# Performance work log

Measured on AMD Instinct MI355X. Metric: run time of the kernel, lower is better.

Reference implementation:

```python
import jax, jax.numpy as jnp
import numpy as np

EPS = 1e-8

def _gn1(x, w, b):
    # GroupNorm(num_groups=1): normalize each sample over (C, T), per-channel affine.
    mean = jnp.mean(x, axis=(1, 2), keepdims=True)
    var = jnp.mean((x - mean) ** 2, axis=(1, 2), keepdims=True)
    xn = (x - mean) * jax.lax.rsqrt(var + EPS)
    return xn * w[None, :, None] + b[None, :, None]

def _film(h, e, gw, gb, bw, bb):
    # gamma/beta: Linear -> ReLU (dropout is identity in eval), broadcast over time.
    gamma = jax.nn.relu(e @ gw.T + gb)  # [B, C]
    beta = jax.nn.relu(e @ bw.T + bb)   # [B, C]
    return gamma[:, :, None] * h + beta[:, :, None]

def setup_inputs() -> dict:
    key = jax.random.key(0)
    ks = jax.random.split(key, 16)
    B, C, T = 16, 256, 16000
    s = lambda k, shape, scale: jax.random.normal(k, shape, dtype=jnp.float32) * scale
    return {
        "x": s(ks[0], (B, C, T), 1.0),
        "cue": s(ks[1], (B, 512), 1.0),
        "gn_a_w": jnp.ones((C,), jnp.float32), "gn_a_b": jnp.zeros((C,), jnp.float32),
        "gn_n_w": jnp.ones((C,), jnp.float32), "gn_n_b": jnp.zeros((C,), jnp.float32),
        "f1g_w": s(ks[2], (C, 512), 0.04), "f1g_b": jnp.zeros((C,), jnp.float32),
        "f1b_w": s(ks[3], (C, 512), 0.04), "f1b_b": jnp.zeros((C,), jnp.float32),
        "ln1_w": jnp.ones((C,), jnp.float32), "ln1_b": jnp.zeros((C,), jnp.float32),
        "conv1_w": s(ks[4], (128, C), 0.06),
        "cds_w": s(ks[5], (256, 512), 0.04),
        "f2g_w": s(ks[6], (128, 256), 0.06), "f2g_b": jnp.zeros((128,), jnp.float32),
        "f2b_w": s(ks[7], (128, 256), 0.06), "f2b_b": jnp.zeros((128,), jnp.float32),
        "ln2_w": jnp.ones((128,), jnp.float32), "ln2_b": jnp.zeros((128,), jnp.float32),
        "conv2_w": s(ks[8], (256, 128), 0.08),
    }

def reference(x, cue, gn_a_w, gn_a_b, gn_n_w, gn_n_b, f1g_w, f1g_b, f1b_w, f1b_b,
              ln1_w, ln1_b, conv1_w, cds_w, f2g_w, f2g_b, f2b_w, f2b_b,
              ln2_w, ln2_b, conv2_w):
    x = _gn1(x, gn_a_w, gn_a_b)                 # norm_audio (GroupNorm(1, C))
    x = _gn1(x, gn_n_w, gn_n_b)                 # norm (GroupNorm(1, C))
    x = _film(x, cue, f1g_w, f1g_b, f1b_w, f1b_b) + x  # film1 + residual
    x = _gn1(x, ln1_w, ln1_b)                   # layer_norm1
    x = jnp.einsum('bct,oc->bot', x, conv1_w)   # 1x1 Conv1d, no bias -> [B,128,T]
    cue2 = jax.nn.relu(cue @ cds_w.T)           # cue_down_sample2 -> [B,256]
    x = _film(x, cue2, f2g_w, f2g_b, f2b_w, f2b_b) + x  # film2 + residual
    x = _gn1(x, ln2_w, ln2_b)                   # layer_norm2
    x = jnp.einsum('bct,oc->bot', x, conv2_w)   # 1x1 Conv1d -> [B,256,T]
    return x
```

## Files before the change

### kernel.cpp

```cpp
#include <hip/hip_runtime.h>
#include <hip/hip_bf16.h>
#include <hip/hip_fp16.h>

#define T_LEN   16000
#define NB      16
#define NTT     250
#define NTB     125
#define EPSV    1e-8f

typedef _Float16 f16x8 __attribute__((ext_vector_type(8)));
typedef float    f32x4 __attribute__((ext_vector_type(4)));

__device__ __forceinline__ ushort f2h(float f) {
    _Float16 h = (_Float16)f;
    return *(ushort*)&h;
}
__device__ __forceinline__ float f4c(const float4& v, int i) {
    return i == 0 ? v.x : i == 1 ? v.y : i == 2 ? v.z : v.w;
}
__device__ __forceinline__ void gld16(const ushort* g, ushort* l) {
    __builtin_amdgcn_global_load_lds(
        (const __attribute__((address_space(1))) uint*)g,
        (__attribute__((address_space(3))) uint*)l, 16, 0, 0);
}
__device__ __forceinline__ float waveRed64(float v) {
    #pragma unroll
    for (int m = 1; m <= 32; m <<= 1) v += __shfl_xor(v, m, 64);
    return v;
}
__device__ __forceinline__ float4 ntload4(const float* p) {
    f32x4 v = __builtin_nontemporal_load((const f32x4*)p);
    return make_float4(v[0], v[1], v[2], v[3]);
}

__device__ __forceinline__ float blockSum256(float v, float* red)
{
    #pragma unroll
    for (int off = 32; off; off >>= 1) v += __shfl_down(v, off, 64);
    __syncthreads();
    if ((threadIdx.x & 63) == 0) red[threadIdx.x >> 6] = v;
    __syncthreads();
    return red[0] + red[1] + red[2] + red[3];
}

__global__ __launch_bounds__(256) void kP1F(
    const float* __restrict__ x, ushort* __restrict__ Xp,
    float* __restrict__ sp, float* __restrict__ qp,
    const float* __restrict__ cue,
    const float* __restrict__ f1g_w, const float* __restrict__ f1g_b,
    const float* __restrict__ f1b_w, const float* __restrict__ f1b_b,
    const float* __restrict__ cds_w,
    float* __restrict__ G1, float* __restrict__ B1, float* __restrict__ CUE2)
{
    const int bid = blockIdx.x;
    if (bid < 256) {
        const int c = bid;
        const int lane = threadIdx.x & 63, w = threadIdx.x >> 6;
        const float4 wg0 = *(const float4*)(f1g_w + c*512 + lane*8);
        const float4 wg1 = *(const float4*)(f1g_w + c*512 + lane*8 + 4);
        const float4 wb0 = *(const float4*)(f1b_w + c*512 + lane*8);
        const float4 wb1 = *(const float4*)(f1b_w + c*512 + lane*8 + 4);
        const float4 wc0 = *(const float4*)(cds_w + c*512 + lane*8);
        const float4 wc1 = *(const float4*)(cds_w + c*512 + lane*8 + 4);
        #pragma unroll
        for (int bb = 0; bb < 4; ++bb) {
            const int b = w*4 + bb;
            const float4 u0 = *(const float4*)(cue + b*512 + lane*8);
            const float4 u1 = *(const float4*)(cue + b*512 + lane*8 + 4);
            float g = 0.f, bt = 0.f, cv = 0.f;
            #pragma unroll
            for (int i = 0; i < 4; ++i) {
                g  = fmaf(f4c(u0,i), f4c(wg0,i), g);  g  = fmaf(f4c(u1,i), f4c(wg1,i), g);
                bt = fmaf(f4c(u0,i), f4c(wb0,i), bt); bt = fmaf(f4c(u1,i), f4c(wb1,i), bt);
                cv = fmaf(f4c(u0,i), f4c(wc0,i), cv); cv = fmaf(f4c(u1,i), f4c(wc1,i), cv);
            }
            g = waveRed64(g); bt = waveRed64(bt); cv = waveRed64(cv);
            if (lane == 0) {
                G1[b*256 + c]   = fmaxf(g + f1g_b[c], 0.f) + 1.f;
                B1[b*256 + c]   = fmaxf(bt + f1b_b[c], 0.f);
                CUE2[b*256 + c] = fmaxf(cv, 0.f);
            }
        }
        return;
    }

    const int pb = bid - 256;
    const int b = pb / NTT, tt = pb % NTT;
    const int t0 = tt * 64;
    const int tid = threadIdx.x;
    const int cq = tid >> 2, jq = tid & 3;
    __shared__ __align__(16) ushort Hs[256][68];

    #pragma unroll
    for (int cc = 0; cc < 4; ++cc) {
        const int c = cc*64 + cq;
        float s4 = 0.f, q4 = 0.f;
        #pragma unroll
        for (int i = 0; i < 4; ++i) {
            const int ts = (jq + i*4)*4;
            const float4 v = ntload4(x + ((size_t)(b*256 + c))*T_LEN + t0 + ts);
            s4 += v.x + v.y + v.z + v.w;
            q4 += v.x*v.x + v.y*v.y + v.z*v.z + v.w*v.w;
            const ushort h0 = f2h(v.x), h1 = f2h(v.y), h2 = f2h(v.z), h3 = f2h(v.w);
            uint2 pk;
            pk.x = (uint)h0 | ((uint)h1 << 16);
            pk.y = (uint)h2 | ((uint)h3 << 16);
            *(uint2*)&Hs[c][ts] = pk;
        }
        s4 += __shfl_xor(s4, 1, 4); s4 += __shfl_xor(s4, 2, 4);
        q4 += __shfl_xor(q4, 1, 4); q4 += __shfl_xor(q4, 2, 4);
        if (jq == 0) {
            sp[((size_t)b*NTT + tt)*256 + c] = s4;
            qp[((size_t)b*NTT + tt)*256 + c] = q4;
        }
    }
    __syncthreads();
    ushort* dst = Xp + ((size_t)(b*NTT + tt)*4)*4096;
    #pragma unroll
    for (int k = 0; k < 8; ++k) {
        const int d  = tid + k*256;
        const int kc = d >> 9, r = d & 511;
        const int t  = r >> 3, us = r & 7;
        const int u  = us ^ (t & 7);
        const int c0 = kc*64 + u*8;
        uint4 val;
        val.x = (uint)Hs[c0+0][t] | ((uint)Hs[c0+1][t] << 16);
        val.y = (uint)Hs[c0+2][t] | ((uint)Hs[c0+3][t] << 16);
        val.z = (uint)Hs[c0+4][t] | ((uint)Hs[c0+5][t] << 16);
        val.w = (uint)Hs[c0+6][t] | ((uint)Hs[c0+7][t] << 16);
        *(uint4*)(dst + (size_t)d*8) = val;
    }
}

__global__ __launch_bounds__(256) void kR_reduce(
    const float* __restrict__ sp, const float* __restrict__ qp,
    float* __restrict__ s1, float* __restrict__ q1)
{
    const int cg = blockIdx.x, b = blockIdx.y;
    const int ci = threadIdx.x & 31, ig = threadIdx.x >> 5;
    const int c = cg*32 + ci;
    float s = 0.f, q = 0.f;
    for (int i = ig; i < NTT; i += 8) {
        s += sp[((size_t)b*NTT + i)*256 + c];
        q += qp[((size_t)b*NTT + i)*256 + c];
    }
    __shared__ float rs[8][32], rq[8][32];
    rs[ig][ci] = s; rq[ig][ci] = q;
    __syncthreads();
    if (threadIdx.x < 32) {
        float ss = 0.f, qq = 0.f;
        #pragma unroll
        for (int g = 0; g < 8; ++g) { ss += rs[g][threadIdx.x]; qq += rq[g][threadIdx.x]; }
        s1[b*256 + cg*32 + threadIdx.x] = ss;
        q1[b*256 + cg*32 + threadIdx.x] = qq;
    }
}

__global__ __launch_bounds__(256) void kM2F(
    const float* __restrict__ s1, const float* __restrict__ q1,
    const float* __restrict__ gn_a_w, const float* __restrict__ gn_a_b,
    const float* __restrict__ gn_n_w, const float* __restrict__ gn_n_b,
    const float* __restrict__ G1, const float* __restrict__ B1,
    const float* __restrict__ ln1_w, const float* __restrict__ ln1_b,
    const float* __restrict__ CUE2,
    const float* __restrict__ f2g_w, const float* __restrict__ f2g_b,
    const float* __restrict__ f2b_w, const float* __restrict__ f2b_b,
    const float* __restrict__ conv1_w,
    float* __restrict__ a4o, float* __restrict__ G2,
    float* __restrict__ E, ushort* __restrict__ Msf)
{
    const int og = blockIdx.x, b = blockIdx.y;
    const int c = threadIdx.x;
    __shared__ float red[4];
    __shared__ float sc2[256], sa4[256], sd4[256], sg2[16];

    const float sc = s1[b*256 + c];
    const float qc = q1[b*256 + c];

    const float Ninv = 1.f / (256.f * 16000.f);
    const float Tf = 16000.f;

    float S  = blockSum256(sc, red);
    float Q  = blockSum256(qc, red);
    float mu1 = S * Ninv;
    float var1 = Q * Ninv - mu1 * mu1;
    float r1 = rsqrtf(var1 + EPSV);
    float a1 = gn_a_w[c] * r1;
    float d1 = gn_a_b[c] - mu1 * r1 * gn_a_w[c];

    float S2 = blockSum256(a1*sc + Tf*d1, red);
    float Q2 = blockSum256(a1*a1*qc + 2.f*a1*d1*sc + Tf*d1*d1, red);
    float mu2 = S2 * Ninv;
    float var2 = Q2 * Ninv - mu2 * mu2;
    float r2 = rsqrtf(var2 + EPSV);
    float wn = gn_n_w[c];
    float a2 = wn * r2 * a1;
    float d2 = wn * r2 * (d1 - mu2) + gn_n_b[c];

    const float g1v = G1[b*256 + c];
    const float b1v = B1[b*256 + c];
    float a3 = g1v * a2;
    float d3 = g1v * d2 + b1v;

    float S3 = blockSum256(a3*sc + Tf*d3, red);
    float Q3 = blockSum256(a3*a3*qc + 2.f*a3*d3*sc + Tf*d3*d3, red);
    float mu3 = S3 * Ninv;
    float var3 = Q3 * Ninv - mu3 * mu3;
    float r3 = rsqrtf(var3 + EPSV);
    float w1 = ln1_w[c];
    const float a4v = w1 * r3 * a3;
    const float d4v = w1 * r3 * (d3 - mu3) + ln1_b[c];
    sa4[c] = a4v;
    sd4[c] = d4v;
    if (og == 0) a4o[b*256 + c] = a4v;
    sc2[c] = CUE2[b*256 + c];
    __syncthreads();

    const int oi = c >> 4, l16 = c & 15;
    const int o = og*16 + oi;
    float g = 0.f, bt = 0.f, ed = 0.f;
    #pragma unroll
    for (int q = 0; q < 4; ++q) {
        const int k0 = l16*16 + q*4;
        const float4 a  = *(const float4*)(f2g_w  + o*256 + k0);
        const float4 bb = *(const float4*)(f2b_w  + o*256 + k0);
        const float4 cc = *(const float4*)(conv1_w + o*256 + k0);
        const float4 u  = *(const float4*)(&sc2[k0]);
        const float4 dd = *(const float4*)(&sd4[k0]);
        #pragma unroll
        for (int i = 0; i < 4; ++i) {
            g  = fmaf(f4c(u,i),  f4c(a,i),  g);
            bt = fmaf(f4c(u,i),  f4c(bb,i), bt);
            ed = fmaf(f4c(dd,i), f4c(cc,i), ed);
        }
    }
    #pragma unroll
    for (int m = 1; m <= 8; m <<= 1) {
        g  += __shfl_xor(g, m, 16);
        bt += __shfl_xor(bt, m, 16);
        ed += __shfl_xor(ed, m, 16);
    }
    if (l16 == 0) {
        const float G2v = fmaxf(g + f2g_b[o], 0.f) + 1.f;
        const float B2v = fmaxf(bt + f2b_b[o], 0.f);
        G2[b*128 + o] = G2v;
        E[b*128 + o]  = G2v * ed + B2v;
        sg2[oi] = G2v;
    }
    __syncthreads();
    const float av = sa4[c];
    #pragma unroll
    for (int i = 0; i < 16; ++i) {
        const int oo = og*16 + i;
        Msf[((size_t)b*128 + oo)*256 + c] = f2h(sg2[i] * conv1_w[oo*256 + c] * av);
    }
}

__global__ __launch_bounds__(256) void kC_gemm(
    const ushort* __restrict__ Xp, const ushort* __restrict__ Msf,
    const float* __restrict__ E,
    float* __restrict__ q2p)
{
    const int tb = blockIdx.x, b = blockIdx.y;
    const int tid = threadIdx.x, lane = tid & 63, w = tid >> 6;
    const int wo = w >> 1, wt = w & 1;
    const int sub = lane >> 4, li = lane & 15;
    const int o0 = wo * 64;
    __shared__ __align__(16) ushort Bs[32768];
    __shared__ float sQp[2][128];

    const ushort* src = Xp + ((size_t)(b*NTT + 2*tb)*4)*4096;
    const ushort* mp  = Msf + (size_t)b*128*256;

    f32x4 acc[4][4];
    #pragma unroll
    for (int i = 0; i < 4; ++i)
        #pragma unroll
        for (int jx = 0; jx < 4; ++jx) acc[i][jx] = (f32x4){0.f,0.f,0.f,0.f};

    #pragma unroll
    for (int m = 0; m < 16; ++m) {
        const int off = m*2048 + w*512;
        gld16(src + off + lane*8, &Bs[off]);
    }
    __syncthreads();

    #pragma unroll
    for (int ks = 0; ks < 8; ++ks) {
        const int kc = ks >> 1;
        const int uo = (ks & 1)*4 + sub;
        f16x8 xf[4];
        #pragma unroll
        for (int ft = 0; ft < 4; ++ft) {
            const int tl = ft*16 + li;
            xf[ft] = *(const f16x8*)&Bs[(wt*4 + kc)*4096 + tl*64 + (uo ^ (tl & 7))*8];
        }
        const int k8 = kc*64 + (ks & 1)*32 + 8*sub;
        #pragma unroll
        for (int fo = 0; fo < 4; ++fo) {
            const f16x8 mf = *(const f16x8*)(mp + (size_t)(o0 + fo*16 + li)*256 + k8);
            #pragma unroll
            for (int ft = 0; ft < 4; ++ft)
                acc[ft][fo] = __builtin_amdgcn_mfma_f32_16x16x32_f16(xf[ft], mf, acc[ft][fo], 0, 0, 0);
        }
    }

    #pragma unroll
    for (int fo = 0; fo < 4; ++fo) {
        const int o = o0 + fo*16 + li;
        const float ev = E[b*128 + o];
        float qv = 0.f;
        #pragma unroll
        for (int ft = 0; ft < 4; ++ft)
            #pragma unroll
            for (int r = 0; r < 4; ++r) {
                const float z = acc[ft][fo][r] + ev;
                qv += z*z;
            }
        qv += __shfl_xor(qv, 16, 64); qv += __shfl_xor(qv, 32, 64);
        if (sub == 0) sQp[wt][o] = qv;
    }
    __syncthreads();
    if (tid < 128)
        q2p[((size_t)b*NTB + tb)*128 + tid] = sQp[0][tid] + sQp[1][tid];
}

__global__ __launch_bounds__(256) void kD2_buildF(
    const float* __restrict__ q2p,
    const float* __restrict__ ln2_w, const float* __restrict__ ln2_b,
    const float* __restrict__ Ev,
    const float* __restrict__ a4, const float* __restrict__ G2,
    const float* __restrict__ s1,
    const float* __restrict__ conv1_w, const float* __restrict__ conv2_w,
    ushort* __restrict__ Fsf, float* __restrict__ h)
{
    const int b = blockIdx.y, pg = blockIdx.x;
    const int tid = threadIdx.x;
    __shared__ float Qs[32][128];
    __shared__ float sA2[128], sAE[128], sAS[256];
    __shared__ float rS[2], rQ[2];

    sAS[tid] = a4[b*256 + tid] * s1[b*256 + tid];
    __syncthreads();

    float s2v = 0.f, qq = 0.f;
    if (tid < 128) {
        float dot = 0.f;
        #pragma unroll 4
        for (int c4 = 0; c4 < 64; ++c4) {
            const float4 cw = *(const float4*)(conv1_w + tid*256 + c4*4);
            const float4 as = *(const float4*)(&sAS[c4*4]);
            dot = fmaf(cw.x, as.x, dot); dot = fmaf(cw.y, as.y, dot);
            dot = fmaf(cw.z, as.z, dot); dot = fmaf(cw.w, as.w, dot);
        }
        s2v = G2[b*128 + tid] * dot + 16000.f * Ev[b*128 + tid];
        for (int tb = 0; tb < NTB; ++tb)
            qq += q2p[((size_t)b*NTB + tb)*128 + tid];
        float S = s2v, Q = qq;
        #pragma unroll
        for (int off = 32; off; off >>= 1) {
            S += __shfl_down(S, off, 64);
            Q += __shfl_down(Q, off, 64);
        }
        if ((tid & 63) == 0) { rS[tid >> 6] = S; rQ[tid >> 6] = Q; }
    }
    __syncthreads();
    const float N2inv = 1.f / (128.f * 16000.f);
    const float mu  = (rS[0] + rS[1]) * N2inv;
    const float var = (rQ[0] + rQ[1]) * N2inv - mu * mu;
    const float r = rsqrtf(var + EPSV);
    if (tid < 128) {
        const float a2v = ln2_w[tid] * r;
        const float d2v = ln2_b[tid] - mu * ln2_w[tid] * r;
        sA2[tid] = a2v;
        sAE[tid] = a2v * Ev[b*128 + tid] + d2v;
    }
    __syncthreads();

    #pragma unroll
    for (int k = 0; k < 16; ++k) {
        const int idx = tid + k*256;
        const int p = idx >> 7, o = idx & 127;
        Qs[p][o] = conv2_w[(pg*32 + p)*128 + o] * sA2[o] * G2[b*128 + o];
    }
    __syncthreads();
    float acc[32];
    #pragma unroll
    for (int p = 0; p < 32; ++p) acc[p] = 0.f;
    for (int o = 0; o < 128; ++o) {
        const float mv = conv1_w[o*256 + tid];
        #pragma unroll
        for (int p = 0; p < 32; ++p) acc[p] = fmaf(Qs[p][o], mv, acc[p]);
    }
    const float a = a4[b*256 + tid];
    #pragma unroll
    for (int p = 0; p < 32; ++p) {
        const size_t idx = ((size_t)b*256 + pg*32 + p)*256 + tid;
        Fsf[idx] = f2h(acc[p] * a);
    }
    if (tid < 32) {
        const int p = pg*32 + tid;
        float hv = 0.f;
        for (int o = 0; o < 128; ++o)
            hv += conv2_w[p*128 + o] * sAE[o];
        h[b*256 + p] = hv;
    }
}

__global__ __launch_bounds__(256) void kE_gemm(
    const ushort* __restrict__ Xp, const ushort* __restrict__ Fsf,
    const float* __restrict__ h, float* __restrict__ out)
{
    const int txp = blockIdx.x;
    const int b = blockIdx.y >> 1;
    const int o_base = (blockIdx.y & 1) * 128;
    const int tid = threadIdx.x, lane = tid & 63, w = tid >> 6;
    const int sub = lane >> 4, li = lane & 15;
    const int o0 = o_base + w * 32;
    __shared__ __align__(16) ushort Bs[2][16384];

    const ushort* fp = Fsf + (size_t)b*65536;

    f16x8 ff[8][2];
    #pragma unroll
    for (int ks = 0; ks < 8; ++ks) {
        const int k8 = (ks >> 1)*64 + (ks & 1)*32 + 8*sub;
        #pragma unroll
        for (int fo = 0; fo < 2; ++fo)
            ff[ks][fo] = *(const f16x8*)(fp + (size_t)(o0 + fo*16 + li)*256 + k8);
    }
    float hv[2];
    #pragma unroll
    for (int fo = 0; fo < 2; ++fo)
        hv[fo] = h[b*256 + o0 + fo*16 + li];

    const ushort* src0 = Xp + ((size_t)(b*NTT + 2*txp)*4)*4096;

    #pragma unroll
    for (int m = 0; m < 8; ++m) {
        const int off = m*2048 + w*512;
        gld16(src0 + off + lane*8, &Bs[0][off]);
    }
    __syncthreads();

    #pragma unroll
    for (int tile = 0; tile < 2; ++tile) {
        if (tile == 0) {
            const ushort* src1 = src0 + 16384;
            #pragma unroll
            for (int m = 0; m < 8; ++m) {
                const int off = m*2048 + w*512;
                gld16(src1 + off + lane*8, &Bs[1][off]);
            }
        }
        f32x4 acc[4][2];
        #pragma unroll
        for (int i = 0; i < 4; ++i)
            #pragma unroll
            for (int jx = 0; jx < 2; ++jx) acc[i][jx] = (f32x4){0.f,0.f,0.f,0.f};

        #pragma unroll
        for (int ks = 0; ks < 8; ++ks) {
            const int kc = ks >> 1;
            const int uo = (ks & 1)*4 + sub;
            f16x8 xf[4];
            #pragma unroll
            for (int ft = 0; ft < 4; ++ft) {
                const int tl = ft*16 + li;
                xf[ft] = *(const f16x8*)&Bs[tile][kc*4096 + tl*64 + (uo ^ (tl & 7))*8];
            }
            #pragma unroll
            for (int fo = 0; fo < 2; ++fo)
                #pragma unroll
                for (int ft = 0; ft < 4; ++ft)
                    acc[ft][fo] = __builtin_amdgcn_mfma_f32_16x16x32_f16(xf[ft], ff[ks][fo], acc[ft][fo], 0, 0, 0);
        }

        const int t0 = (2*txp + tile)*64;
        #pragma unroll
        for (int fo = 0; fo < 2; ++fo) {
            const int o = o0 + fo*16 + li;
            float* obase = out + ((size_t)(b*256 + o))*T_LEN + t0;
            #pragma unroll
            for (int ft = 0; ft < 4; ++ft) {
                f32x4 v;
                v[0] = acc[ft][fo][0] + hv[fo];
                v[1] = acc[ft][fo][1] + hv[fo];
                v[2] = acc[ft][fo][2] + hv[fo];
                v[3] = acc[ft][fo][3] + hv[fo];
                __builtin_nontemporal_store(v, (f32x4*)(obase + ft*16 + sub*4));
            }
        }
        if (tile == 0) __syncthreads();
    }
}

extern "C" void kernel_launch(void* const* d_in, const int* in_sizes, int n_in,
                              void* d_out, int out_size, void* d_ws, size_t ws_size,
                              hipStream_t stream)
{
    const float* x       = (const float*)d_in[0];
    const float* cue     = (const float*)d_in[1];
    const float* gn_a_w  = (const float*)d_in[2];
    const float* gn_a_b  = (const float*)d_in[3];
    const float* gn_n_w  = (const float*)d_in[4];
    const float* gn_n_b  = (const float*)d_in[5];
    const float* f1g_w   = (const float*)d_in[6];
    const float* f1g_b   = (const float*)d_in[7];
    const float* f1b_w   = (const float*)d_in[8];
    const float* f1b_b   = (const float*)d_in[9];
    const float* ln1_w   = (const float*)d_in[10];
    const float* ln1_b   = (const float*)d_in[11];
    const float* conv1_w = (const float*)d_in[12];
    const float* cds_w   = (const float*)d_in[13];
    const float* f2g_w   = (const float*)d_in[14];
    const float* f2g_b   = (const float*)d_in[15];
    const float* f2b_w   = (const float*)d_in[16];
    const float* f2b_b   = (const float*)d_in[17];
    const float* ln2_w   = (const float*)d_in[18];
    const float* ln2_b   = (const float*)d_in[19];
    const float* conv2_w = (const float*)d_in[20];
    float* out = (float*)d_out;

    float* ws = (float*)d_ws;
    float*  sp   = ws;
    float*  qp   = ws + 1024000;
    float*  G1   = ws + 2048000;
    float*  B1   = ws + 2052096;
    float*  CUE2 = ws + 2056192;
    float*  G2   = ws + 2060288;
    float*  a4   = ws + 2062336;
    float*  E    = ws + 2066432;
    float*  h    = ws + 2068480;
    float*  s1   = ws + 2072576;
    float*  q1   = ws + 2076672;
    float*  q2p  = ws + 2080768;
    ushort* Msf  = (ushort*)(ws + 2336768);
    ushort* Fsf  = (ushort*)(ws + 2598912);
    ushort* Xp   = (ushort*)(ws + 3123200);

    kP1F<<<256 + NTT*NB, 256, 0, stream>>>(x, Xp, sp, qp,
        cue, f1g_w, f1g_b, f1b_w, f1b_b, cds_w, G1, B1, CUE2);

    kR_reduce<<<dim3(8, NB), 256, 0, stream>>>(sp, qp, s1, q1);

    kM2F<<<dim3(8, NB), 256, 0, stream>>>(s1, q1,
        gn_a_w, gn_a_b, gn_n_w, gn_n_b, G1, B1, ln1_w, ln1_b,
        CUE2, f2g_w, f2g_b, f2b_w, f2b_b, conv1_w,
        a4, G2, E, Msf);

    kC_gemm<<<dim3(NTB, NB), 256, 0, stream>>>(Xp, Msf, E, q2p);

    kD2_buildF<<<dim3(8, NB), 256, 0, stream>>>(q2p, ln2_w, ln2_b, E,
                                                a4, G2, s1, conv1_w, conv2_w,
                                                Fsf, h);

    kE_gemm<<<dim3(NTB, NB*2), 256, 0, stream>>>(Xp, Fsf, h, out);
}
```

Baseline: 293.2 us.

## Keep GEMM weights in registers and double-buffer two X tiles in kC_gemm

kC_gemm now gives each wave 32 output channels across both time tiles instead of 64 channels on one tile. The wave preloads its whole Msf weight slice into registers once rather than reloading it per k-step from global memory. The second 64-step X tile is loaded into a separate LDS buffer while the first is computed, and the per-wave partial sums are written straight to q2p without the shared reduction. This trades more register pressure (16 f16x8 weight vectors held live) for fewer global weight loads and overlap of the second tile's load with compute.

Measured after the change: 271.3 us. 7.5% less time.

```diff
diff --git a/kernel.cpp b/kernel.cpp
--- a/kernel.cpp
+++ b/kernel.cpp
@@ -261,68 +261,90 @@
     const float* __restrict__ E,
     float* __restrict__ q2p)
 {
-    const int tb = blockIdx.x, b = blockIdx.y;
+    const int tp = blockIdx.x, b = blockIdx.y;
     const int tid = threadIdx.x, lane = tid & 63, w = tid >> 6;
-    const int wo = w >> 1, wt = w & 1;
     const int sub = lane >> 4, li = lane & 15;
-    const int o0 = wo * 64;
-    __shared__ __align__(16) ushort Bs[32768];
-    __shared__ float sQp[2][128];
-
-    const ushort* src = Xp + ((size_t)(b*NTT + 2*tb)*4)*4096;
-    const ushort* mp  = Msf + (size_t)b*128*256;
-
-    f32x4 acc[4][4];
-    #pragma unroll
-    for (int i = 0; i < 4; ++i)
-        #pragma unroll
-        for (int jx = 0; jx < 4; ++jx) acc[i][jx] = (f32x4){0.f,0.f,0.f,0.f};
-
-    #pragma unroll
-    for (int m = 0; m < 16; ++m) {
+    const int o0 = w * 32;
+    __shared__ __align__(16) ushort Bs[2][16384];
+
+    const ushort* mp = Msf + (size_t)b*32768;
+
+    f16x8 mf[8][2];
+    #pragma unroll
+    for (int ks = 0; ks < 8; ++ks) {
+        const int k8 = (ks >> 1)*64 + (ks & 1)*32 + 8*sub;
+        #pragma unroll
+        for (int fo = 0; fo < 2; ++fo)
+            mf[ks][fo] = *(const f16x8*)(mp + (size_t)(o0 + fo*16 + li)*256 + k8);
+    }
+    float ev[2];
+    #pragma unroll
+    for (int fo = 0; fo < 2; ++fo)
+        ev[fo] = E[b*128 + o0 + fo*16 + li];
+
+    const ushort* src0 = Xp + ((size_t)(b*NTT + 2*tp)*4)*4096;
+
+    #pragma unroll
+    for (int m = 0; m < 8; ++m) {
         const int off = m*2048 + w*512;
-        gld16(src + off + lane*8, &Bs[off]);
-    }
-    __syncthreads();
-
-    #pragma unroll
-    for (int ks = 0; ks < 8; ++ks) {
-        const int kc = ks >> 1;
-        const int uo = (ks & 1)*4 + sub;
-        f16x8 xf[4];
-        #pragma unroll
-        for (int ft = 0; ft < 4; ++ft) {
-            const int tl = ft*16 + li;
-            xf[ft] = *(const f16x8*)&Bs[(wt*4 + kc)*4096 + tl*64 + (uo ^ (tl & 7))*8];
-        }
-        const int k8 = kc*64 + (ks & 1)*32 + 8*sub;
-        #pragma unroll
-        for (int fo = 0; fo < 4; ++fo) {
-            const f16x8 mf = *(const f16x8*)(mp + (size_t)(o0 + fo*16 + li)*256 + k8);
+        gld16(src0 + off + lane*8, &Bs[0][off]);
+    }
+    __syncthreads();
+
+    float qv[2] = {0.f, 0.f};
+    #pragma unroll
+    for (int tile = 0; tile < 2; ++tile) {
+        if (tile == 0) {
+            const ushort* src1 = src0 + 16384;
+            #pragma unroll
+            for (int m = 0; m < 8; ++m) {
+                const int off = m*2048 + w*512;
+                gld16(src1 + off + lane*8, &Bs[1][off]);
+            }
+        }
+        f32x4 acc[4][2];
+        #pragma unroll
+        for (int i = 0; i < 4; ++i)
+            #pragma unroll
+            for (int jx = 0; jx < 2; ++jx) acc[i][jx] = (f32x4){0.f,0.f,0.f,0.f};
+
+        #pragma unroll
+        for (int ks = 0; ks < 8; ++ks) {
+            const int kc = ks >> 1;
+            const int uo = (ks & 1)*4 + sub;
+            f16x8 xf[4];
+            #pragma unroll
+            for (int ft = 0; ft < 4; ++ft) {
+                const int tl = ft*16 + li;
+                xf[ft] = *(const f16x8*)&Bs[tile][kc*4096 + tl*64 + (uo ^ (tl & 7))*8];
+            }
+            #pragma unroll
+            for (int fo = 0; fo < 2; ++fo)
+                #pragma unroll
+                for (int ft = 0; ft < 4; ++ft)
+                    acc[ft][fo] = __builtin_amdgcn_mfma_f32_16x16x32_f16(xf[ft], mf[ks][fo], acc[ft][fo], 0, 0, 0);
+        }
+
+        #pragma unroll
+        for (int fo = 0; fo < 2; ++fo)
             #pragma unroll
             for (int ft = 0; ft < 4; ++ft)
-                acc[ft][fo] = __builtin_amdgcn_mfma_f32_16x16x32_f16(xf[ft], mf, acc[ft][fo], 0, 0, 0);
-        }
-    }
-
-    #pragma unroll
-    for (int fo = 0; fo < 4; ++fo) {
-        const int o = o0 + fo*16 + li;
-        const float ev = E[b*128 + o];
-        float qv = 0.f;
-        #pragma unroll
-        for (int ft = 0; ft < 4; ++ft)
-            #pragma unroll
-            for (int r = 0; r < 4; ++r) {
-                const float z = acc[ft][fo][r] + ev;
-                qv += z*z;
-            }
-        qv += __shfl_xor(qv, 16, 64); qv += __shfl_xor(qv, 32, 64);
-        if (sub == 0) sQp[wt][o] = qv;
-    }
-    __syncthreads();
-    if (tid < 128)
-        q2p[((size_t)b*NTB + tb)*128 + tid] = sQp[0][tid] + sQp[1][tid];
+                #pragma unroll
+                for (int r = 0; r < 4; ++r) {
+                    const float z = acc[ft][fo][r] + ev[fo];
+                    qv[fo] += z*z;
+                }
+        if (tile == 0) __syncthreads();
+    }
+
+    #pragma unroll
+    for (int fo = 0; fo < 2; ++fo) {
+        float q = qv[fo];
+        q += __shfl_xor(q, 16, 64);
+        q += __shfl_xor(q, 32, 64);
+        if (sub == 0)
+            q2p[((size_t)b*NTB + tp)*128 + o0 + fo*16 + li] = q;
+    }
 }
 
 __global__ __launch_bounds__(256) void kD2_buildF(
```
